# Kernel tuning notes

Hardware: AMD Instinct MI355X
Metric: run time of the kernel (lower is better)

The kernel has to match this reference:

```python
import jax, jax.numpy as jnp
import numpy as np

N = 100000      # nodes
E = 3200000     # edges (avg degree 32)
IN = 256        # in_features
OUT = 128       # out_features


def setup_inputs() -> dict:
    key = jax.random.key(0)
    k_x, k_r, k_c, k_v, k_w, k_b = jax.random.split(key, 6)
    x = jax.random.normal(k_x, (N, IN), dtype=jnp.float32)
    row = jax.random.randint(k_r, (E,), 0, N)          # destination node of each edge
    col = jax.random.randint(k_c, (E,), 0, N)          # source node of each edge
    adj_vals = jax.random.uniform(k_v, (E,), dtype=jnp.float32)  # sparse adj values
    stdv = 1.0 / np.sqrt(OUT)                          # matches reset_parameters
    weight = jax.random.uniform(k_w, (IN, OUT), dtype=jnp.float32, minval=-stdv, maxval=stdv)
    bias = jax.random.uniform(k_b, (OUT,), dtype=jnp.float32, minval=-stdv, maxval=stdv)
    return {"x": x, "adj_vals": adj_vals, "weight": weight, "bias": bias,
            "row": row, "col": col}


def reference(x, adj_vals, weight, bias, row, col):
    # support = input @ W                       [N, OUT]
    support = x @ weight
    # output = spmm(adj, support): for each edge (r, c, v): out[r] += v * support[c]
    gathered = adj_vals[:, None] * support[col]  # [E, OUT] irregular gather
    out = jax.ops.segment_sum(gathered, row, num_segments=N)  # [N, OUT] scatter-add
    return out + bias
```

## Files before the change

### kernel.cpp

```cpp
#include <hip/hip_runtime.h>

#define INF 256
#define OUTF 128
#define RB 512
#define NBMAX 256
#define BUCKET_CAP 17408

typedef _Float16 half8 __attribute__((ext_vector_type(8)));
typedef float f32x4 __attribute__((ext_vector_type(4)));

__device__ inline unsigned short f16bits(float v) {
    union { unsigned short u; _Float16 h; } cv;
    cv.h = (_Float16)v;
    return cv.u;
}
__device__ inline float f16val15(unsigned rec) {
    union { unsigned short u; _Float16 h; } cv;
    cv.u = (unsigned short)(rec << 1);
    return (float)cv.h;
}

__global__ __launch_bounds__(256) void k_prepack(const float* __restrict__ w,
                                                 _Float16* __restrict__ wpack,
                                                 int* __restrict__ bcursor,
                                                 int NB) {
    int t = blockIdx.x * 256 + threadIdx.x;
    int k = t >> 7, n = t & 127;
    int ks = k >> 5, quad = (k >> 3) & 3, j = k & 7;
    int ct = n >> 4, nn = n & 15;
    wpack[(((ks * 8 + ct) * 4 + quad) * 16 + nn) * 8 + j] = (_Float16)w[k * OUTF + n];
    if (t < NB) bcursor[t] = t * BUCKET_CAP;
}

__global__ __launch_bounds__(256) void gcn_gemm_mfma(const float* __restrict__ x,
                                                     const _Float16* __restrict__ wpack,
                                                     _Float16* __restrict__ support,
                                                     int N) {
    const int tid = threadIdx.x;
    const int wv = tid >> 6;
    const int lane = tid & 63;
    const int m16 = lane & 15;
    const int quad = lane >> 4;
    const int rowbase = blockIdx.x * 128 + wv * 32;

    f32x4 acc[2][8];
#pragma unroll
    for (int rt = 0; rt < 2; ++rt)
#pragma unroll
        for (int ct = 0; ct < 8; ++ct)
            acc[rt][ct] = (f32x4){0.f, 0.f, 0.f, 0.f};

    int r0 = rowbase + m16;
    int r1 = rowbase + 16 + m16;
    int r0c = (r0 < N) ? r0 : N - 1;
    int r1c = (r1 < N) ? r1 : N - 1;
    const float* xr0 = x + (long)r0c * INF + quad * 8;
    const float* xr1 = x + (long)r1c * INF + quad * 8;

    for (int ks = 0; ks < 8; ++ks) {
        float4 u0 = *(const float4*)(xr0 + ks * 32);
        float4 v0 = *(const float4*)(xr0 + ks * 32 + 4);
        float4 u1 = *(const float4*)(xr1 + ks * 32);
        float4 v1 = *(const float4*)(xr1 + ks * 32 + 4);
        half8 a0 = {(_Float16)u0.x, (_Float16)u0.y, (_Float16)u0.z, (_Float16)u0.w,
                    (_Float16)v0.x, (_Float16)v0.y, (_Float16)v0.z, (_Float16)v0.w};
        half8 a1 = {(_Float16)u1.x, (_Float16)u1.y, (_Float16)u1.z, (_Float16)u1.w,
                    (_Float16)v1.x, (_Float16)v1.y, (_Float16)v1.z, (_Float16)v1.w};

        half8 b[8];
#pragma unroll
        for (int ct = 0; ct < 8; ++ct)
            b[ct] = *(const half8*)(wpack + (size_t)(((ks * 8 + ct) * 4 + quad) * 16 + m16) * 8);

#pragma unroll
        for (int ct = 0; ct < 8; ++ct) {
            acc[0][ct] = __builtin_amdgcn_mfma_f32_16x16x32_f16(a0, b[ct], acc[0][ct], 0, 0, 0);
            acc[1][ct] = __builtin_amdgcn_mfma_f32_16x16x32_f16(a1, b[ct], acc[1][ct], 0, 0, 0);
        }
    }

#pragma unroll
    for (int rt = 0; rt < 2; ++rt) {
        int rb = rowbase + rt * 16 + quad * 4;
#pragma unroll
        for (int reg = 0; reg < 4; ++reg) {
            int r = rb + reg;
            if (r < N) {
#pragma unroll
                for (int ct = 0; ct < 8; ++ct)
                    support[(long)r * OUTF + ct * 16 + m16] = (_Float16)acc[rt][ct][reg];
            }
        }
    }
}

__global__ __launch_bounds__(256) void k_coarse_scatter(const int* __restrict__ row,
                                                        const int* __restrict__ col,
                                                        const float* __restrict__ vals,
                                                        int* __restrict__ bcursor,
                                                        uint2* __restrict__ tmp,
                                                        int NB, int E) {
    __shared__ int cnt[NBMAX];
    __shared__ int sbase[NBMAX];
    const int tid = threadIdx.x;
    if (tid < NBMAX) cnt[tid] = 0;
    __syncthreads();

    int b[16], rk[16];
    uint2 rec[16];
    const int base4 = blockIdx.x * 1024;
#pragma unroll
    for (int j = 0; j < 4; ++j) {
        int e4 = base4 + j * 256 + tid;
        if (e4 * 4 < E) {
            int4   r4 = ((const int4*)row)[e4];
            int4   c4 = ((const int4*)col)[e4];
            float4 v4 = ((const float4*)vals)[e4];
            int rr[4] = {r4.x, r4.y, r4.z, r4.w};
            int cc[4] = {c4.x, c4.y, c4.z, c4.w};
            float vv[4] = {v4.x, v4.y, v4.z, v4.w};
#pragma unroll
            for (int s = 0; s < 4; ++s) {
                int idx = j * 4 + s;
                rec[idx].x = ((unsigned)rr[s] << 15) | ((unsigned)f16bits(vv[s]) >> 1);
                rec[idx].y = (unsigned)cc[s];
                b[idx] = rr[s] >> 9;
                rk[idx] = atomicAdd(&cnt[b[idx]], 1);
            }
        } else {
#pragma unroll
            for (int s = 0; s < 4; ++s) b[j * 4 + s] = -1;
        }
    }
    __syncthreads();
    if (tid < NB) {
        int c = cnt[tid];
        if (c) sbase[tid] = atomicAdd(&bcursor[tid], c);
    }
    __syncthreads();
#pragma unroll
    for (int j = 0; j < 16; ++j) {
        if (b[j] >= 0) tmp[sbase[b[j]] + rk[j]] = rec[j];
    }
}

__global__ __launch_bounds__(1024) void k_bucket_sort(const uint2* __restrict__ tmp,
                                                      const int* __restrict__ bcursor,
                                                      unsigned* __restrict__ frecs,
                                                      int* __restrict__ rs,
                                                      int* __restrict__ re,
                                                      int N) {
    __shared__ int cnt[RB];
    __shared__ int offs[RB];

    const int tid = threadIdx.x;
    const int b = blockIdx.x;
    const int start = b * BUCKET_CAP;
    int n = bcursor[b] - start;
    if (n > BUCKET_CAP) n = BUCKET_CAP;
    const int row0 = b * RB;

    if (tid < RB) cnt[tid] = 0;
    __syncthreads();

    for (int i = tid; i < n; i += 1024) {
        uint2 r = tmp[start + i];
        atomicAdd(&cnt[(r.x >> 15) & (RB - 1)], 1);
    }
    __syncthreads();

    if (tid < RB) offs[tid] = cnt[tid];
    __syncthreads();
    for (int d = 1; d < RB; d <<= 1) {
        int add = (tid < RB && tid >= d) ? offs[tid - d] : 0;
        __syncthreads();
        if (tid < RB) offs[tid] += add;
        __syncthreads();
    }
    if (tid < RB) {
        int excl = offs[tid] - cnt[tid];
        offs[tid] = excl;
        int r = row0 + tid;
        if (r < N) {
            rs[r] = start + excl;
            re[r] = start + excl + cnt[tid];
        }
    }
    __syncthreads();

    for (int i = tid; i < n; i += 1024) {
        uint2 r = tmp[start + i];
        int lr = (r.x >> 15) & (RB - 1);
        int pos = atomicAdd(&offs[lr], 1);
        frecs[start + pos] = (r.y << 15) | (r.x & 0x7FFF);
    }
}

__global__ __launch_bounds__(256) void k_gather(const _Float16* __restrict__ sup,
                                                const unsigned* __restrict__ frecs,
                                                const int* __restrict__ rs,
                                                const int* __restrict__ re,
                                                const float* __restrict__ bias,
                                                float* __restrict__ out,
                                                int N) {
    int wid = (blockIdx.x * 256 + threadIdx.x) >> 6;
    int lane = threadIdx.x & 63;
    if (wid >= N) return;

    const int q = lane >> 4;
    const int fl = lane & 15;
    const unsigned fb = (unsigned)fl << 4;
    const char* supb = (const char*)sup;

    int i = rs[wid];
    const int end = re[wid];

    float a0 = 0.f, a1 = 0.f, a2 = 0.f, a3 = 0.f;
    float a4 = 0.f, a5 = 0.f, a6 = 0.f, a7 = 0.f;

    for (; i + 32 <= end; i += 32) {
#pragma unroll
        for (int k = 0; k < 8; ++k) {
            unsigned rec = frecs[i + 4 * k + q];
            float v = f16val15(rec);
            half8 h = *(const half8*)(supb + (((rec & 0xFFFF8000u) >> 7) + fb));
            a0 += v * (float)h[0]; a1 += v * (float)h[1];
            a2 += v * (float)h[2]; a3 += v * (float)h[3];
            a4 += v * (float)h[4]; a5 += v * (float)h[5];
            a6 += v * (float)h[6]; a7 += v * (float)h[7];
        }
    }
    for (; i + 16 <= end; i += 16) {
#pragma unroll
        for (int k = 0; k < 4; ++k) {
            unsigned rec = frecs[i + 4 * k + q];
            float v = f16val15(rec);
            half8 h = *(const half8*)(supb + (((rec & 0xFFFF8000u) >> 7) + fb));
            a0 += v * (float)h[0]; a1 += v * (float)h[1];
            a2 += v * (float)h[2]; a3 += v * (float)h[3];
            a4 += v * (float)h[4]; a5 += v * (float)h[5];
            a6 += v * (float)h[6]; a7 += v * (float)h[7];
        }
    }
    for (; i < end; i += 4) {
        int idx = i + q;
        unsigned rec = frecs[(idx < end) ? idx : (end - 1)];
        float v = (idx < end) ? f16val15(rec) : 0.f;
        half8 h = *(const half8*)(supb + (((rec & 0xFFFF8000u) >> 7) + fb));
        a0 += v * (float)h[0]; a1 += v * (float)h[1];
        a2 += v * (float)h[2]; a3 += v * (float)h[3];
        a4 += v * (float)h[4]; a5 += v * (float)h[5];
        a6 += v * (float)h[6]; a7 += v * (float)h[7];
    }

    a0 += __shfl_xor(a0, 16); a0 += __shfl_xor(a0, 32);
    a1 += __shfl_xor(a1, 16); a1 += __shfl_xor(a1, 32);
    a2 += __shfl_xor(a2, 16); a2 += __shfl_xor(a2, 32);
    a3 += __shfl_xor(a3, 16); a3 += __shfl_xor(a3, 32);
    a4 += __shfl_xor(a4, 16); a4 += __shfl_xor(a4, 32);
    a5 += __shfl_xor(a5, 16); a5 += __shfl_xor(a5, 32);
    a6 += __shfl_xor(a6, 16); a6 += __shfl_xor(a6, 32);
    a7 += __shfl_xor(a7, 16); a7 += __shfl_xor(a7, 32);

    if (q == 0) {
        float4 b0 = ((const float4*)bias)[fl * 2];
        float4 b1 = ((const float4*)bias)[fl * 2 + 1];
        float4 o0 = {a0 + b0.x, a1 + b0.y, a2 + b0.z, a3 + b0.w};
        float4 o1 = {a4 + b1.x, a5 + b1.y, a6 + b1.z, a7 + b1.w};
        float4* orow = (float4*)(out + (long)wid * OUTF);
        orow[fl * 2] = o0;
        orow[fl * 2 + 1] = o1;
    }
}

extern "C" void kernel_launch(void* const* d_in, const int* in_sizes, int n_in,
                              void* d_out, int out_size, void* d_ws, size_t ws_size,
                              hipStream_t stream) {
    const float* x    = (const float*)d_in[0];
    const float* vals = (const float*)d_in[1];
    const float* w    = (const float*)d_in[2];
    const float* bias = (const float*)d_in[3];
    const int*   row  = (const int*)d_in[4];
    const int*   col  = (const int*)d_in[5];

    const int N = in_sizes[0] / INF;
    const int E = in_sizes[1];
    const int NB = (N + RB - 1) / RB;

    char* p = (char*)d_ws;
    _Float16* support = (_Float16*)p;  p += (size_t)N * OUTF * sizeof(_Float16);
    unsigned* frecs   = (unsigned*)p;  p += (size_t)NB * BUCKET_CAP * sizeof(unsigned);
    _Float16* wpack   = (_Float16*)p;  p += (size_t)INF * OUTF * sizeof(_Float16);
    int* rs           = (int*)p;       p += (size_t)N * sizeof(int);
    int* re           = (int*)p;       p += (size_t)N * sizeof(int);
    int* bcursor      = (int*)p;       p += (size_t)NBMAX * sizeof(int);

    uint2* tmp = (uint2*)d_out;

    const int EB = (E + 4095) / 4096;

    k_prepack<<<(INF * OUTF) / 256, 256, 0, stream>>>(w, wpack, bcursor, NB);

    gcn_gemm_mfma<<<(N + 127) / 128, 256, 0, stream>>>(x, wpack, support, N);

    k_coarse_scatter<<<EB, 256, 0, stream>>>(row, col, vals, bcursor, tmp, NB, E);

    k_bucket_sort<<<NB, 1024, 0, stream>>>(tmp, bcursor, frecs, rs, re, N);

    {
        int blocks = (N * 64 + 255) / 256;
        k_gather<<<blocks, 256, 0, stream>>>(support, frecs, rs, re, bias,
                                             (float*)d_out, N);
    }
}
```

Measured before the change: 380.8 us.

## Split gather feature dimension across two wavefronts per row

Each destination row is now handled by two wavefronts, each covering half of the 128 output features (64 halfs, 128 bytes), with 8 edges processed in parallel per wavefront instead of 4. Block indices are interleaved so the two halves of a row group launch in adjacent blocks, which should help the shared support rows hit in cache. This doubles the number of waves, which adds parallelism for low-degree rows and brings more loads into flight. In exchange the edge records are read twice, an extra shuffle-reduction stage is needed, and the unroll depth drops from 32 to 16 edges.

After: 374.7 us. No clear change (-1.6%).

```diff
diff --git a/kernel.cpp b/kernel.cpp
--- a/kernel.cpp
+++ b/kernel.cpp
@@ -203,13 +203,17 @@
                                                 const float* __restrict__ bias,
                                                 float* __restrict__ out,
                                                 int N) {
-    int wid = (blockIdx.x * 256 + threadIdx.x) >> 6;
-    int lane = threadIdx.x & 63;
+    const int g = blockIdx.x;
+    const int h = (g >> 2) & 1;
+    const int j = (g >> 3) * 4 + (g & 3);
+    const int wv = threadIdx.x >> 6;
+    const int lane = threadIdx.x & 63;
+    const int wid = j * 4 + wv;
     if (wid >= N) return;
 
-    const int q = lane >> 4;
-    const int fl = lane & 15;
-    const unsigned fb = (unsigned)fl << 4;
+    const int q = lane >> 3;
+    const int fl = lane & 7;
+    const unsigned fb = (unsigned)(h * 128 + fl * 16);
     const char* supb = (const char*)sup;
 
     int i = rs[wid];
@@ -218,58 +222,47 @@
     float a0 = 0.f, a1 = 0.f, a2 = 0.f, a3 = 0.f;
     float a4 = 0.f, a5 = 0.f, a6 = 0.f, a7 = 0.f;
 
-    for (; i + 32 <= end; i += 32) {
-#pragma unroll
-        for (int k = 0; k < 8; ++k) {
-            unsigned rec = frecs[i + 4 * k + q];
+    for (; i + 16 <= end; i += 16) {
+#pragma unroll
+        for (int k = 0; k < 2; ++k) {
+            unsigned rec = frecs[i + 8 * k + q];
             float v = f16val15(rec);
-            half8 h = *(const half8*)(supb + (((rec & 0xFFFF8000u) >> 7) + fb));
-            a0 += v * (float)h[0]; a1 += v * (float)h[1];
-            a2 += v * (float)h[2]; a3 += v * (float)h[3];
-            a4 += v * (float)h[4]; a5 += v * (float)h[5];
-            a6 += v * (float)h[6]; a7 += v * (float)h[7];
-        }
-    }
-    for (; i + 16 <= end; i += 16) {
-#pragma unroll
-        for (int k = 0; k < 4; ++k) {
-            unsigned rec = frecs[i + 4 * k + q];
-            float v = f16val15(rec);
-            half8 h = *(const half8*)(supb + (((rec & 0xFFFF8000u) >> 7) + fb));
-            a0 += v * (float)h[0]; a1 += v * (float)h[1];
-            a2 += v * (float)h[2]; a3 += v * (float)h[3];
-            a4 += v * (float)h[4]; a5 += v * (float)h[5];
-            a6 += v * (float)h[6]; a7 += v * (float)h[7];
-        }
-    }
-    for (; i < end; i += 4) {
+            half8 hh = *(const half8*)(supb + (((rec & 0xFFFF8000u) >> 7) + fb));
+            a0 += v * (float)hh[0]; a1 += v * (float)hh[1];
+            a2 += v * (float)hh[2]; a3 += v * (float)hh[3];
+            a4 += v * (float)hh[4]; a5 += v * (float)hh[5];
+            a6 += v * (float)hh[6]; a7 += v * (float)hh[7];
+        }
+    }
+    for (; i < end; i += 8) {
         int idx = i + q;
         unsigned rec = frecs[(idx < end) ? idx : (end - 1)];
         float v = (idx < end) ? f16val15(rec) : 0.f;
-        half8 h = *(const half8*)(supb + (((rec & 0xFFFF8000u) >> 7) + fb));
-        a0 += v * (float)h[0]; a1 += v * (float)h[1];
-        a2 += v * (float)h[2]; a3 += v * (float)h[3];
-        a4 += v * (float)h[4]; a5 += v * (float)h[5];
-        a6 += v * (float)h[6]; a7 += v * (float)h[7];
-    }
-
-    a0 += __shfl_xor(a0, 16); a0 += __shfl_xor(a0, 32);
-    a1 += __shfl_xor(a1, 16); a1 += __shfl_xor(a1, 32);
-    a2 += __shfl_xor(a2, 16); a2 += __shfl_xor(a2, 32);
-    a3 += __shfl_xor(a3, 16); a3 += __shfl_xor(a3, 32);
-    a4 += __shfl_xor(a4, 16); a4 += __shfl_xor(a4, 32);
-    a5 += __shfl_xor(a5, 16); a5 += __shfl_xor(a5, 32);
-    a6 += __shfl_xor(a6, 16); a6 += __shfl_xor(a6, 32);
-    a7 += __shfl_xor(a7, 16); a7 += __shfl_xor(a7, 32);
+        half8 hh = *(const half8*)(supb + (((rec & 0xFFFF8000u) >> 7) + fb));
+        a0 += v * (float)hh[0]; a1 += v * (float)hh[1];
+        a2 += v * (float)hh[2]; a3 += v * (float)hh[3];
+        a4 += v * (float)hh[4]; a5 += v * (float)hh[5];
+        a6 += v * (float)hh[6]; a7 += v * (float)hh[7];
+    }
+
+    a0 += __shfl_xor(a0, 8); a0 += __shfl_xor(a0, 16); a0 += __shfl_xor(a0, 32);
+    a1 += __shfl_xor(a1, 8); a1 += __shfl_xor(a1, 16); a1 += __shfl_xor(a1, 32);
+    a2 += __shfl_xor(a2, 8); a2 += __shfl_xor(a2, 16); a2 += __shfl_xor(a2, 32);
+    a3 += __shfl_xor(a3, 8); a3 += __shfl_xor(a3, 16); a3 += __shfl_xor(a3, 32);
+    a4 += __shfl_xor(a4, 8); a4 += __shfl_xor(a4, 16); a4 += __shfl_xor(a4, 32);
+    a5 += __shfl_xor(a5, 8); a5 += __shfl_xor(a5, 16); a5 += __shfl_xor(a5, 32);
+    a6 += __shfl_xor(a6, 8); a6 += __shfl_xor(a6, 16); a6 += __shfl_xor(a6, 32);
+    a7 += __shfl_xor(a7, 8); a7 += __shfl_xor(a7, 16); a7 += __shfl_xor(a7, 32);
 
     if (q == 0) {
-        float4 b0 = ((const float4*)bias)[fl * 2];
-        float4 b1 = ((const float4*)bias)[fl * 2 + 1];
+        const float* bh = bias + h * 64 + fl * 8;
+        float4 b0 = *(const float4*)(bh);
+        float4 b1 = *(const float4*)(bh + 4);
         float4 o0 = {a0 + b0.x, a1 + b0.y, a2 + b0.z, a3 + b0.w};
         float4 o1 = {a4 + b1.x, a5 + b1.y, a6 + b1.z, a7 + b1.w};
-        float4* orow = (float4*)(out + (long)wid * OUTF);
-        orow[fl * 2] = o0;
-        orow[fl * 2 + 1] = o1;
+        float* orow = out + (long)wid * OUTF + h * 64 + fl * 8;
+        *(float4*)(orow) = o0;
+        *(float4*)(orow + 4) = o1;
     }
 }
 
@@ -308,7 +301,8 @@
     k_bucket_sort<<<NB, 1024, 0, stream>>>(tmp, bcursor, frecs, rs, re, N);
 
     {
-        int blocks = (N * 64 + 255) / 256;
+        int rowquads = (N + 3) / 4;
+        int blocks = 2 * rowquads;
         k_gather<<<blocks, 256, 0, stream>>>(support, frecs, rs, re, bias,
                                              (float*)d_out, N);
     }
```
